# Performance work log

Hardware: AMD Instinct MI355X
Metric: run time of the kernel (lower is better)

## Reference

```python
import jax, jax.numpy as jnp
import numpy as np

N_QUBITS = 4
N_LAYERS = 2
BATCH = 262144


def _apply_ry(psi, theta, wire):
    # psi: (B, 2,2,2,2) real statevector; theta: scalar or (B,)
    c = jnp.reshape(jnp.cos(theta * 0.5), (-1, 1, 1, 1))
    s = jnp.reshape(jnp.sin(theta * 0.5), (-1, 1, 1, 1))
    psi = jnp.moveaxis(psi, wire + 1, 1)
    a, b = psi[:, 0], psi[:, 1]
    psi = jnp.stack([c * a - s * b, s * a + c * b], axis=1)
    return jnp.moveaxis(psi, 1, wire + 1)


def _apply_cnot(psi, ctrl, tgt):
    # flip target amplitude where control bit is 1
    psi = jnp.moveaxis(psi, (ctrl + 1, tgt + 1), (1, 2))
    psi = psi.at[:, 1].set(psi[:, 1, ::-1])
    return jnp.moveaxis(psi, (1, 2), (ctrl + 1, tgt + 1))


def _circuit(encoded, q_params):
    # Batched 4-qubit statevector sim (RY/CNOT are real matrices -> real psi).
    B = encoded.shape[0]
    psi = jnp.zeros((B, 2 ** N_QUBITS), encoded.dtype).at[:, 0].set(1.0)
    psi = psi.reshape((B,) + (2,) * N_QUBITS)  # wire 0 = most significant axis
    for w in range(N_QUBITS):
        psi = _apply_ry(psi, encoded[:, w], w)
    for layer in range(N_LAYERS):
        for i in range(N_QUBITS - 1):
            psi = _apply_cnot(psi, i, i + 1)
        psi = _apply_cnot(psi, N_QUBITS - 1, 0)  # ring closure (n_qubits > 2)
        for i in range(N_QUBITS):
            psi = _apply_ry(psi, q_params[layer * N_QUBITS + i], i)
    p = psi * psi  # probabilities
    zs = []
    for w in range(N_QUBITS):
        pw = jnp.moveaxis(p, w + 1, 1).reshape(B, 2, -1)
        zs.append(pw[:, 0].sum(-1) - pw[:, 1].sum(-1))  # <Z_w>
    return jnp.stack(zs, axis=-1)  # (B, 4)


def setup_inputs() -> dict:
    key = jax.random.key(0)
    ks = jax.random.split(key, 10)
    f32 = jnp.float32
    state = jax.random.normal(ks[0], (BATCH, 64), dtype=f32)
    # state_encoder: Linear(64,32) -> ReLU -> Linear(32,4) -> Tanh
    W1 = jax.random.normal(ks[1], (32, 64), dtype=f32) / np.sqrt(64.0)
    b1 = jnp.zeros((32,), f32)
    W2 = jax.random.normal(ks[2], (N_QUBITS, 32), dtype=f32) / np.sqrt(32.0)
    b2 = jnp.zeros((N_QUBITS,), f32)
    q_params = jax.random.normal(ks[3], (N_LAYERS * N_QUBITS,), dtype=f32) * 0.1
    # q_value_head: Linear(4,32) -> ReLU -> Linear(32,16) -> Tanh
    H1 = jax.random.normal(ks[4], (32, N_QUBITS), dtype=f32) / np.sqrt(float(N_QUBITS))
    c1 = jnp.zeros((32,), f32)
    H2 = jax.random.normal(ks[5], (16, 32), dtype=f32) / np.sqrt(32.0)
    c2 = jnp.zeros((16,), f32)
    return {"state": state, "W1": W1, "b1": b1, "W2": W2, "b2": b2,
            "q_params": q_params, "H1": H1, "c1": c1, "H2": H2, "c2": c2}


def reference(state, W1, b1, W2, b2, q_params, H1, c1, H2, c2):
    B = state.shape[0]
    x = state.reshape(B, -1)
    h = jax.nn.relu(x @ W1.T + b1)
    encoded = jnp.tanh(h @ W2.T + b2)            # (B, 4) rotation angles
    qf = _circuit(encoded, q_params)             # (B, 4) PauliZ expectations
    h2 = jax.nn.relu(qf @ H1.T + c1)
    q_values = jnp.tanh(h2 @ H2.T + c2)          # (B, 16)
    return q_values.reshape(B, 4, 4)
```

## Files before the change

kernel.cpp:

```cpp
#include <hip/hip_runtime.h>
#include <hip/hip_bf16.h>

#define TPB 256
#define BATCH 262144

__device__ __forceinline__ float fast_tanh(float x) {
    float ax = fabsf(x);
    float e  = __expf(-2.0f * ax);
    float t  = (1.0f - e) * __builtin_amdgcn_rcpf(1.0f + e);
    return copysignf(t, x);
}

template <int MASK>
__device__ __forceinline__ void ry_gate(float* psi, float c, float s) {
#pragma unroll
    for (int i = 0; i < 16; i++) {
        if (!(i & MASK)) {
            float a = psi[i], b = psi[i | MASK];
            psi[i]        = c * a - s * b;
            psi[i | MASK] = s * a + c * b;
        }
    }
}

template <int CM, int TM>
__device__ __forceinline__ void cnot_gate(float* psi) {
#pragma unroll
    for (int i = 0; i < 16; i++) {
        if ((i & CM) && !(i & TM)) {
            float t = psi[i];
            psi[i] = psi[i | TM];
            psi[i | TM] = t;
        }
    }
}

__global__ __launch_bounds__(TPB, 4) void qnet_kernel(
    const float* __restrict__ state,
    const float* __restrict__ W1, const float* __restrict__ b1,
    const float* __restrict__ W2, const float* __restrict__ b2,
    const float* __restrict__ qp,
    const float* __restrict__ H1, const float* __restrict__ c1,
    const float* __restrict__ H2, const float* __restrict__ c2,
    float* __restrict__ out)
{
    const int bidx = blockIdx.x * TPB + threadIdx.x;

    const float4* x4 = reinterpret_cast<const float4*>(state + (size_t)bidx * 64);
    float x[64];
#pragma unroll
    for (int k = 0; k < 16; k++) {
        float4 v = x4[k];
        x[k * 4 + 0] = v.x; x[k * 4 + 1] = v.y;
        x[k * 4 + 2] = v.z; x[k * 4 + 3] = v.w;
    }

    float h[32];
#pragma unroll
    for (int j = 0; j < 32; j++) {
        float acc = b1[j];
#pragma unroll
        for (int k = 0; k < 64; k++)
            acc = fmaf(x[k], W1[j * 64 + k], acc);
        h[j] = fmaxf(acc, 0.0f);
    }

    float e[4];
#pragma unroll
    for (int w = 0; w < 4; w++) {
        float acc = b2[w];
#pragma unroll
        for (int k = 0; k < 32; k++)
            acc = fmaf(h[k], W2[w * 32 + k], acc);
        e[w] = fast_tanh(acc);
    }

    float qf[4];
    {
        float psi[16];
#pragma unroll
        for (int i = 0; i < 16; i++) psi[i] = 0.0f;
        psi[0] = 1.0f;

        float s, c;
        __sincosf(0.5f * e[0], &s, &c); ry_gate<8>(psi, c, s);
        __sincosf(0.5f * e[1], &s, &c); ry_gate<4>(psi, c, s);
        __sincosf(0.5f * e[2], &s, &c); ry_gate<2>(psi, c, s);
        __sincosf(0.5f * e[3], &s, &c); ry_gate<1>(psi, c, s);

#pragma unroll
        for (int layer = 0; layer < 2; layer++) {
            cnot_gate<8, 4>(psi);
            cnot_gate<4, 2>(psi);
            cnot_gate<2, 1>(psi);
            cnot_gate<1, 8>(psi);
#pragma unroll
            for (int i = 0; i < 4; i++) {
                float s2, c2;
                __sincosf(0.5f * qp[layer * 4 + i], &s2, &c2);
                if (i == 0) ry_gate<8>(psi, c2, s2);
                if (i == 1) ry_gate<4>(psi, c2, s2);
                if (i == 2) ry_gate<2>(psi, c2, s2);
                if (i == 3) ry_gate<1>(psi, c2, s2);
            }
        }

        float p[16];
#pragma unroll
        for (int i = 0; i < 16; i++) p[i] = psi[i] * psi[i];
#pragma unroll
        for (int w = 0; w < 4; w++) {
            const int m = 8 >> w;
            float z = 0.0f;
#pragma unroll
            for (int i = 0; i < 16; i++) z += (i & m) ? -p[i] : p[i];
            qf[w] = z;
        }
    }

    float h2[32];
#pragma unroll
    for (int j = 0; j < 32; j++) {
        float a = c1[j];
        a = fmaf(qf[0], H1[j * 4 + 0], a);
        a = fmaf(qf[1], H1[j * 4 + 1], a);
        a = fmaf(qf[2], H1[j * 4 + 2], a);
        a = fmaf(qf[3], H1[j * 4 + 3], a);
        h2[j] = fmaxf(a, 0.0f);
    }

    float qv[16];
#pragma unroll
    for (int o = 0; o < 16; o++) {
        float acc = c2[o];
#pragma unroll
        for (int k = 0; k < 32; k++)
            acc = fmaf(h2[k], H2[o * 32 + k], acc);
        qv[o] = fast_tanh(acc);
    }

    float4* dst = reinterpret_cast<float4*>(out + (size_t)bidx * 16);
#pragma unroll
    for (int k = 0; k < 4; k++) {
        dst[k] = make_float4(qv[k * 4 + 0], qv[k * 4 + 1],
                             qv[k * 4 + 2], qv[k * 4 + 3]);
    }
}

extern "C" void kernel_launch(void* const* d_in, const int* in_sizes, int n_in,
                              void* d_out, int out_size, void* d_ws, size_t ws_size,
                              hipStream_t stream) {
    const float* state = (const float*)d_in[0];
    const float* W1    = (const float*)d_in[1];
    const float* b1    = (const float*)d_in[2];
    const float* W2    = (const float*)d_in[3];
    const float* b2    = (const float*)d_in[4];
    const float* qp    = (const float*)d_in[5];
    const float* H1    = (const float*)d_in[6];
    const float* c1    = (const float*)d_in[7];
    const float* H2    = (const float*)d_in[8];
    const float* c2    = (const float*)d_in[9];
    float* out = (float*)d_out;

    const int blocks = BATCH / TPB;
    qnet_kernel<<<blocks, TPB, 0, stream>>>(state, W1, b1, W2, b2, qp,
                                            H1, c1, H2, c2, out);
}
```

Baseline: 138.1 us.

## Run encoder and value-head linear layers on fp16 MFMA with LDS redistribution

The 64->32 encoder layer and the 32->16 value-head layer move from per-thread scalar FMA loops to wave-level 16x16x32 fp16 MFMA instructions. Inputs and weights are converted to fp16 on load, and results are redistributed per row through a padded shared-memory buffer. This targets the dominant per-thread FMA cost and the large register footprint of holding 64 inputs per thread. In exchange it adds fp16 rounding of the activations and weights, block-level barriers, a 34 KB shared buffer that may limit occupancy, and scalar output stores in place of float4 stores.

Measured after the change: 119.8 us. 1.15x faster.

```diff
diff --git a/kernel.cpp b/kernel.cpp
--- a/kernel.cpp
+++ b/kernel.cpp
@@ -3,6 +3,10 @@
 
 #define TPB 256
 #define BATCH 262144
+#define S 34
+
+typedef _Float16 half8_t __attribute__((ext_vector_type(8)));
+typedef float    f32x4   __attribute__((ext_vector_type(4)));
 
 __device__ __forceinline__ float fast_tanh(float x) {
     float ax = fabsf(x);
@@ -33,6 +37,13 @@
             psi[i | TM] = t;
         }
     }
+}
+
+__device__ __forceinline__ half8_t cvt8(float4 a, float4 b) {
+    half8_t r;
+    r[0] = (_Float16)a.x; r[1] = (_Float16)a.y; r[2] = (_Float16)a.z; r[3] = (_Float16)a.w;
+    r[4] = (_Float16)b.x; r[5] = (_Float16)b.y; r[6] = (_Float16)b.z; r[7] = (_Float16)b.w;
+    return r;
 }
 
 __global__ __launch_bounds__(TPB, 4) void qnet_kernel(
@@ -44,35 +55,70 @@
     const float* __restrict__ H2, const float* __restrict__ c2,
     float* __restrict__ out)
 {
-    const int bidx = blockIdx.x * TPB + threadIdx.x;
-
-    const float4* x4 = reinterpret_cast<const float4*>(state + (size_t)bidx * 64);
-    float x[64];
-#pragma unroll
-    for (int k = 0; k < 16; k++) {
-        float4 v = x4[k];
-        x[k * 4 + 0] = v.x; x[k * 4 + 1] = v.y;
-        x[k * 4 + 2] = v.z; x[k * 4 + 3] = v.w;
-    }
+    __shared__ float sh[4 * 64 * S];
+
+    const int tid  = threadIdx.x;
+    const int lane = tid & 63;
+    const int wv   = tid >> 6;
+    const int l15  = lane & 15;
+    const int lq   = lane >> 4;
+    const int rowBase = blockIdx.x * TPB + wv * 64;
+    float* hb = sh + wv * 64 * S;
+
+    half8_t bW1[2][2];
+#pragma unroll
+    for (int u = 0; u < 2; u++)
+#pragma unroll
+        for (int kt = 0; kt < 2; kt++) {
+            const float* p = W1 + (16 * u + l15) * 64 + 32 * kt + lq * 8;
+            bW1[u][kt] = cvt8(*(const float4*)p, *(const float4*)(p + 4));
+        }
+    const float bias0 = b1[l15];
+    const float bias1 = b1[16 + l15];
+
+    f32x4 acc[4][2];
+#pragma unroll
+    for (int mt = 0; mt < 4; mt++)
+#pragma unroll
+        for (int u = 0; u < 2; u++)
+#pragma unroll
+            for (int r = 0; r < 4; r++) acc[mt][u][r] = 0.0f;
+
+#pragma unroll
+    for (int kt = 0; kt < 2; kt++) {
+#pragma unroll
+        for (int mt = 0; mt < 4; mt++) {
+            const float* p = state + (size_t)(rowBase + 16 * mt + l15) * 64 + 32 * kt + lq * 8;
+            half8_t a = cvt8(*(const float4*)p, *(const float4*)(p + 4));
+            acc[mt][0] = __builtin_amdgcn_mfma_f32_16x16x32_f16(a, bW1[0][kt], acc[mt][0], 0, 0, 0);
+            acc[mt][1] = __builtin_amdgcn_mfma_f32_16x16x32_f16(a, bW1[1][kt], acc[mt][1], 0, 0, 0);
+        }
+    }
+
+#pragma unroll
+    for (int mt = 0; mt < 4; mt++)
+#pragma unroll
+        for (int r = 0; r < 4; r++) {
+            int row = 16 * mt + 4 * lq + r;
+            hb[row * S + l15]      = fmaxf(acc[mt][0][r] + bias0, 0.0f);
+            hb[row * S + 16 + l15] = fmaxf(acc[mt][1][r] + bias1, 0.0f);
+        }
+    __syncthreads();
 
     float h[32];
-#pragma unroll
-    for (int j = 0; j < 32; j++) {
-        float acc = b1[j];
-#pragma unroll
-        for (int k = 0; k < 64; k++)
-            acc = fmaf(x[k], W1[j * 64 + k], acc);
-        h[j] = fmaxf(acc, 0.0f);
+    {
+        const float2* hr = reinterpret_cast<const float2*>(hb + lane * S);
+#pragma unroll
+        for (int j = 0; j < 16; j++) { float2 v = hr[j]; h[2 * j] = v.x; h[2 * j + 1] = v.y; }
     }
 
     float e[4];
 #pragma unroll
     for (int w = 0; w < 4; w++) {
-        float acc = b2[w];
-#pragma unroll
-        for (int k = 0; k < 32; k++)
-            acc = fmaf(h[k], W2[w * 32 + k], acc);
-        e[w] = fast_tanh(acc);
+        float a = b2[w];
+#pragma unroll
+        for (int k = 0; k < 32; k++) a = fmaf(h[k], W2[w * 32 + k], a);
+        e[w] = fast_tanh(a);
     }
 
     float qf[4];
@@ -96,12 +142,12 @@
             cnot_gate<1, 8>(psi);
 #pragma unroll
             for (int i = 0; i < 4; i++) {
-                float s2, c2;
-                __sincosf(0.5f * qp[layer * 4 + i], &s2, &c2);
-                if (i == 0) ry_gate<8>(psi, c2, s2);
-                if (i == 1) ry_gate<4>(psi, c2, s2);
-                if (i == 2) ry_gate<2>(psi, c2, s2);
-                if (i == 3) ry_gate<1>(psi, c2, s2);
+                float s2, c2v;
+                __sincosf(0.5f * qp[layer * 4 + i], &s2, &c2v);
+                if (i == 0) ry_gate<8>(psi, c2v, s2);
+                if (i == 1) ry_gate<4>(psi, c2v, s2);
+                if (i == 2) ry_gate<2>(psi, c2v, s2);
+                if (i == 3) ry_gate<1>(psi, c2v, s2);
             }
         }
 
@@ -129,22 +175,47 @@
         h2[j] = fmaxf(a, 0.0f);
     }
 
-    float qv[16];
-#pragma unroll
-    for (int o = 0; o < 16; o++) {
-        float acc = c2[o];
-#pragma unroll
-        for (int k = 0; k < 32; k++)
-            acc = fmaf(h2[k], H2[o * 32 + k], acc);
-        qv[o] = fast_tanh(acc);
-    }
-
-    float4* dst = reinterpret_cast<float4*>(out + (size_t)bidx * 16);
-#pragma unroll
-    for (int k = 0; k < 4; k++) {
-        dst[k] = make_float4(qv[k * 4 + 0], qv[k * 4 + 1],
-                             qv[k * 4 + 2], qv[k * 4 + 3]);
-    }
+    __syncthreads();
+
+    {
+        float2* hw = reinterpret_cast<float2*>(hb + lane * S);
+#pragma unroll
+        for (int j = 0; j < 16; j++) hw[j] = make_float2(h2[2 * j], h2[2 * j + 1]);
+    }
+    __syncthreads();
+
+    half8_t bH2;
+    {
+        const float* p = H2 + l15 * 32 + lq * 8;
+        bH2 = cvt8(*(const float4*)p, *(const float4*)(p + 4));
+    }
+
+    f32x4 acc2[4];
+#pragma unroll
+    for (int mt = 0; mt < 4; mt++)
+#pragma unroll
+        for (int r = 0; r < 4; r++) acc2[mt][r] = 0.0f;
+
+#pragma unroll
+    for (int mt = 0; mt < 4; mt++) {
+        const float2* q = reinterpret_cast<const float2*>(hb + (16 * mt + l15) * S + lq * 8);
+        float2 a0 = q[0], a1 = q[1], a2 = q[2], a3 = q[3];
+        half8_t a;
+        a[0] = (_Float16)a0.x; a[1] = (_Float16)a0.y;
+        a[2] = (_Float16)a1.x; a[3] = (_Float16)a1.y;
+        a[4] = (_Float16)a2.x; a[5] = (_Float16)a2.y;
+        a[6] = (_Float16)a3.x; a[7] = (_Float16)a3.y;
+        acc2[mt] = __builtin_amdgcn_mfma_f32_16x16x32_f16(a, bH2, acc2[mt], 0, 0, 0);
+    }
+
+    const float cc = c2[l15];
+#pragma unroll
+    for (int mt = 0; mt < 4; mt++)
+#pragma unroll
+        for (int r = 0; r < 4; r++) {
+            int row = rowBase + 16 * mt + 4 * lq + r;
+            out[(size_t)row * 16 + l15] = fast_tanh(acc2[mt][r] + cc);
+        }
 }
 
 extern "C" void kernel_launch(void* const* d_in, const int* in_sizes, int n_in,
```
